# Optimization experiments

Hardware: AMD Instinct MI355X
Metric: run time of the kernel (lower is better)

Reference implementation:

```python
import jax, jax.numpy as jnp
import numpy as np

NUM_EMBEDDINGS = 4096
EMBEDDING_DIM = 512
N_TOKENS = 32768
COMMITMENT_COST = 0.25


def setup_inputs() -> dict:
    key = jax.random.key(0)
    k1, k2 = jax.random.split(key)
    flat_input = jax.random.normal(k1, (N_TOKENS, EMBEDDING_DIM), dtype=jnp.float32)
    # torch init: uniform(-1/K, 1/K)
    weight = jax.random.uniform(k2, (NUM_EMBEDDINGS, EMBEDDING_DIM), dtype=jnp.float32,
                                minval=-1.0 / NUM_EMBEDDINGS, maxval=1.0 / NUM_EMBEDDINGS)
    return {"flat_input": flat_input, "weight": weight}


def reference(flat_input, weight):
    distances = (jnp.sum(flat_input ** 2, axis=1, keepdims=True)
                 + jnp.sum(weight ** 2, axis=1)
                 - 2.0 * jnp.matmul(flat_input, weight.T))
    encoding_indices = jnp.argmin(distances, axis=1)  # [N]
    # one-hot @ weight == direct gather of codebook rows
    quantized = weight[encoding_indices]  # [N, D]

    e_latent_loss = jnp.mean((jax.lax.stop_gradient(quantized) - flat_input) ** 2, axis=1)
    q_latent_loss = jnp.mean((quantized - jax.lax.stop_gradient(flat_input)) ** 2, axis=1)
    loss = q_latent_loss + COMMITMENT_COST * e_latent_loss  # [N]

    # straight-through estimator
    quantized_st = flat_input + jax.lax.stop_gradient(quantized - flat_input)

    # avg_probs = mean of one-hot encodings over batch = normalized code counts
    counts = jnp.zeros((NUM_EMBEDDINGS,), dtype=flat_input.dtype).at[encoding_indices].add(1.0)
    avg_probs = counts / flat_input.shape[0]
    perplexity = jnp.exp(-jnp.sum(avg_probs * jnp.log(avg_probs + 1e-10)))

    return quantized_st, loss, perplexity, encoding_indices
```

## Files before the change

kernel.cpp:

```cpp
#include <hip/hip_runtime.h>
#include <math.h>

#define N_TOK 32768
#define K_CODES 4096
#define DIM 512
#define COMMIT 0.25f
#define NCAND 8
#define NSPLIT 2
#define SPLIT_CODES (K_CODES / NSPLIT)
#define NITER (SPLIT_CODES / 256)
#define BIAS 0.125f

typedef short s16x8 __attribute__((ext_vector_type(8)));
typedef float f32x4 __attribute__((ext_vector_type(4)));
typedef unsigned int uint32;
typedef unsigned long long u64;
typedef unsigned short u16;

__device__ __forceinline__ u16 f2bf(float f) {
    uint32 b = __float_as_uint(f);
    return (u16)((b + 0x7FFFu + ((b >> 16) & 1u)) >> 16);
}

__device__ __forceinline__ void gload16(const u16* g, u16* l) {
    __builtin_amdgcn_global_load_lds(
        (const __attribute__((address_space(1))) void*)g,
        (__attribute__((address_space(3))) void*)l,
        16, 0, 0);
}

__global__ __launch_bounds__(256) void tobf16_kernel(const float* __restrict__ src,
                                                     u16* __restrict__ dst, int n4) {
    int i = blockIdx.x * 256 + threadIdx.x;
    int stride = gridDim.x * 256;
    for (; i < n4; i += stride) {
        float4 v = ((const float4*)src)[i];
        ushort4 o;
        o.x = f2bf(v.x); o.y = f2bf(v.y); o.z = f2bf(v.z); o.w = f2bf(v.w);
        ((ushort4*)dst)[i] = o;
    }
}

__global__ __launch_bounds__(256) void rowsq_np_kernel(const float* __restrict__ a,
                                                       float* __restrict__ out,
                                                       int nrows) {
    #pragma clang fp contract(off)
    const int gw   = (blockIdx.x * 256 + threadIdx.x) >> 6;
    const int lane = threadIdx.x & 63;
    const int row  = gw * 8 + (lane >> 3);
    const int j    = lane & 7;
    if (row >= nrows) return;
    const float* p = a + (size_t)row * DIM;
    float blk[4];
    #pragma unroll
    for (int b = 0; b < 4; ++b) {
        const float* q = p + b * 128;
        float v = q[j];
        float r = v * v;
        for (int i = 8; i < 128; i += 8) { float u = q[i + j]; r += u * u; }
        float s1 = r  + __shfl_xor(r, 1);
        float s2 = s1 + __shfl_xor(s1, 2);
        float s3 = s2 + __shfl_xor(s2, 4);
        blk[b] = s3;
    }
    float res = (blk[0] + blk[1]) + (blk[2] + blk[3]);
    if (j == 0) out[row] = res;
}

__global__ __launch_bounds__(512, 2) void screen_kernel(const u16* __restrict__ xb,
                                                        const u16* __restrict__ wb,
                                                        const float* __restrict__ w2f,
                                                        u64* __restrict__ candPart) {
    __shared__ __attribute__((aligned(16))) u16 POOL[65536];

    const int tid  = threadIdx.x;
    const int wv   = tid >> 6;
    const int wt   = wv >> 1;
    const int wcc  = wv & 1;
    const int lane = tid & 63;
    const int quad = lane >> 4;
    const int n15  = lane & 15;
    const int m0   = blockIdx.x * 256;
    const int sbase = blockIdx.y * SPLIT_CODES;

    const int l8  = lane >> 3;
    const int qsw = (lane & 7) ^ l8;

    const u16* xg = xb + (size_t)(m0 + wv * 32 + l8) * DIM + qsw * 8;
    const u16* wit = wb + (size_t)(sbase + wv * 32 + l8) * DIM + qsw * 8;

    uint32 r1[16], r2[16];
    #pragma unroll
    for (int i = 0; i < 16; ++i) { r1[i] = 0xFFFFFFFFu; r2[i] = 0xFFFFFFFFu; }

    #pragma unroll
    for (int j = 0; j < 4; ++j) {
        gload16(xg + (size_t)(j * 8) * DIM, &POOL[wv * 2048 + j * 512]);
        gload16(wit + (size_t)(j * 8) * DIM, &POOL[32768 + wv * 2048 + j * 512]);
    }
    __syncthreads();

    for (int it = 0; it < NITER; ++it) {
        const int nbase = sbase + it * 256;

        float w2pb[8];
        #pragma unroll
        for (int c = 0; c < 8; ++c) w2pb[c] = w2f[nbase + wcc * 128 + c * 16 + n15] + BIAS;

        f32x4 acc[4][8];
        #pragma unroll
        for (int i = 0; i < 4; ++i)
            #pragma unroll
            for (int c = 0; c < 8; ++c) acc[i][c] = (f32x4){0.f, 0.f, 0.f, 0.f};

        for (int kc = 0; kc < 8; ++kc) {
            if (kc < 7) {
                const int nb = (kc + 1) & 1;
                const int ko = (kc + 1) * 64;
                #pragma unroll
                for (int j = 0; j < 4; ++j) {
                    gload16(xg + (size_t)(j * 8) * DIM + ko,
                            &POOL[nb * 16384 + wv * 2048 + j * 512]);
                    gload16(wit + (size_t)(j * 8) * DIM + ko,
                            &POOL[32768 + nb * 16384 + wv * 2048 + j * 512]);
                }
            } else if (it < NITER - 1) {
                const u16* wn = wit + (size_t)256 * DIM;
                #pragma unroll
                for (int j = 0; j < 4; ++j) {
                    gload16(xg + (size_t)(j * 8) * DIM, &POOL[wv * 2048 + j * 512]);
                    gload16(wn + (size_t)(j * 8) * DIM, &POOL[32768 + wv * 2048 + j * 512]);
                }
            }

            const u16* X = &POOL[(kc & 1) * 16384];
            const u16* W = &POOL[32768 + (kc & 1) * 16384];
            #pragma unroll
            for (int s = 0; s < 2; ++s) {
                const int qoff = ((s * 4 + quad) ^ (n15 & 7)) * 8;
                s16x8 af[4];
                #pragma unroll
                for (int i = 0; i < 4; ++i) {
                    const int tr = wt * 64 + i * 16 + n15;
                    af[i] = *(const s16x8*)&X[tr * 64 + qoff];
                }
                #pragma unroll
                for (int c = 0; c < 8; ++c) {
                    const int cr = wcc * 128 + c * 16 + n15;
                    s16x8 bf = *(const s16x8*)&W[cr * 64 + qoff];
                    #pragma unroll
                    for (int i = 0; i < 4; ++i)
                        acc[i][c] = __builtin_amdgcn_mfma_f32_16x16x32_bf16(af[i], bf, acc[i][c], 0, 0, 0);
                }
            }
            __syncthreads();
        }

        #pragma unroll
        for (int i = 0; i < 4; ++i)
            #pragma unroll
            for (int r = 0; r < 4; ++r) {
                const int ti = i * 4 + r;
                #pragma unroll
                for (int c = 0; c < 8; ++c) {
                    float s = fmaf(-2.0f, acc[i][c][r], w2pb[c]);
                    uint32 key = (__float_as_uint(s) & 0xFFFFFFC0u) | (uint32)((it << 3) | c);
                    uint32 mx = r1[ti] > key ? r1[ti] : key;
                    r1[ti] = r1[ti] < key ? r1[ti] : key;
                    r2[ti] = r2[ti] < mx ? r2[ti] : mx;
                }
            }
        wit += (size_t)256 * DIM;
    }

    u64* MS = (u64*)POOL;
    #pragma unroll
    for (int ti = 0; ti < 16; ++ti) {
        const int i = ti >> 2, r = ti & 3;
        const int tloc = wt * 64 + i * 16 + quad * 4 + r;
        #pragma unroll
        for (int e = 0; e < 2; ++e) {
            uint32 k  = e ? r2[ti] : r1[ti];
            uint32 vb = k & 0xFFFFFFC0u;
            uint32 id = k & 63u;
            uint32 code = (uint32)(sbase + (id >> 3) * 256 + wcc * 128 + (id & 7) * 16 + n15);
            MS[tloc * 64 + (wcc * 16 + n15) * 2 + e] = ((u64)vb << 32) | code;
        }
    }
    __syncthreads();
    if (tid < 256) {
        u64 best[6];
        #pragma unroll
        for (int c = 0; c < 6; ++c) best[c] = 0xFFFFFFFFFFFFFFFFull;
        for (int e = 0; e < 64; ++e) {
            u64 v = MS[tid * 64 + e];
            if (v < best[5]) {
                best[5] = v;
                #pragma unroll
                for (int p = 5; p > 0; --p)
                    if (best[p] < best[p - 1]) { u64 tv = best[p]; best[p] = best[p - 1]; best[p - 1] = tv; }
            }
        }
        const int token = m0 + tid;
        u64* dst = candPart + ((size_t)blockIdx.y * N_TOK + token) * 6;
        #pragma unroll
        for (int c = 0; c < 6; ++c) dst[c] = best[c];
    }
}

__global__ __launch_bounds__(256) void mergecand_kernel(const u64* __restrict__ candPart,
                                                        int* __restrict__ candF) {
    int t = blockIdx.x * 256 + threadIdx.x;
    u64 best[NCAND];
    #pragma unroll
    for (int c = 0; c < NCAND; ++c) best[c] = 0xFFFFFFFFFFFFFFFFull;
    for (int s = 0; s < NSPLIT; ++s) {
        const u64* src = candPart + ((size_t)s * N_TOK + t) * 6;
        #pragma unroll
        for (int c = 0; c < 6; ++c) {
            u64 v = src[c];
            if (v < best[NCAND - 1]) {
                best[NCAND - 1] = v;
                #pragma unroll
                for (int p = NCAND - 1; p > 0; --p)
                    if (best[p] < best[p - 1]) { u64 tv = best[p]; best[p] = best[p - 1]; best[p - 1] = tv; }
            }
        }
    }
    #pragma unroll
    for (int c = 0; c < NCAND; ++c) candF[(size_t)t * NCAND + c] = (int)(best[c] & 0xFFFu);
}

__global__ __launch_bounds__(256) void refine_kernel(const float* __restrict__ x,
                                                     const float* __restrict__ w,
                                                     const float* __restrict__ x2np,
                                                     const float* __restrict__ w2np,
                                                     const int* __restrict__ cand,
                                                     int* __restrict__ idx) {
    const int t    = blockIdx.x * 4 + (threadIdx.x >> 6);
    const int lane = threadIdx.x & 63;

    const float* xr = x + (size_t)t * DIM;
    float xv[8];
    #pragma unroll
    for (int j = 0; j < 8; ++j) xv[j] = xr[lane + 64 * j];
    const float x2 = x2np[t];

    float bd = 3.4e38f;
    int   bk = 0x7fffffff;
    for (int c = 0; c < NCAND; ++c) {
        int k = cand[(size_t)t * NCAND + c];
        const float* wr = w + (size_t)k * DIM;
        double m = 0.0;
        #pragma unroll
        for (int j = 0; j < 8; ++j)
            m = fma((double)xv[j], (double)wr[lane + 64 * j], m);
        #pragma unroll
        for (int off = 32; off >= 1; off >>= 1) m += __shfl_down(m, off);
        if (lane == 0) {
            #pragma clang fp contract(off)
            float m32 = (float)m;
            float T1  = x2 + w2np[k];
            float d   = T1 - 2.0f * m32;
            if (d < bd || (d == bd && k < bk)) { bd = d; bk = k; }
        }
    }
    if (lane == 0) idx[t] = bk;
}

__global__ __launch_bounds__(256) void gather_kernel(const float* __restrict__ x,
                                                     const float* __restrict__ w,
                                                     const int* __restrict__ idx,
                                                     float* __restrict__ out_q,
                                                     float* __restrict__ out_loss,
                                                     float* __restrict__ out_ind,
                                                     int* __restrict__ counts) {
    const int wave = threadIdx.x >> 6;
    const int lane = threadIdx.x & 63;
    const int token = blockIdx.x * 4 + wave;
    const int k = idx[token];

    const float4* xr = (const float4*)(x + (size_t)token * DIM);
    const float4* wr = (const float4*)(w + (size_t)k * DIM);
    float4*       qo = (float4*)(out_q + (size_t)token * DIM);

    float ss = 0.f;
    #pragma unroll
    for (int j = 0; j < 2; ++j) {
        int e = lane + j * 64;
        float4 xv = xr[e];
        float4 wv = wr[e];
        float4 d, o;
        d.x = wv.x - xv.x; o.x = xv.x + d.x;
        d.y = wv.y - xv.y; o.y = xv.y + d.y;
        d.z = wv.z - xv.z; o.z = xv.z + d.z;
        d.w = wv.w - xv.w; o.w = xv.w + d.w;
        ss += d.x * d.x + d.y * d.y + d.z * d.z + d.w * d.w;
        qo[e] = o;
    }
    #pragma unroll
    for (int off = 32; off >= 1; off >>= 1) ss += __shfl_down(ss, off);
    if (lane == 0) {
        float lm = ss * (1.0f / DIM);
        out_loss[token] = lm + COMMIT * lm;
        out_ind[token] = (float)k;
        atomicAdd(&counts[k], 1);
    }
}

__global__ __launch_bounds__(256) void perplex_kernel(const int* __restrict__ counts,
                                                      float* __restrict__ out2) {
    __shared__ double red[4];
    const int tid = threadIdx.x;
    const int lane = tid & 63;
    const int wid = tid >> 6;
    double s = 0.0;
    for (int t = tid; t < K_CODES; t += 256) {
        int c = counts[t];
        if (c) {
            double p = (double)c * (1.0 / N_TOK);
            s += p * log(p + 1e-10);
        }
    }
    #pragma unroll
    for (int off = 32; off >= 1; off >>= 1) s += __shfl_down(s, off);
    if (lane == 0) red[wid] = s;
    __syncthreads();
    if (tid == 0) {
        double t = red[0] + red[1] + red[2] + red[3];
        out2[0] = (float)exp(-t);
    }
}

extern "C" void kernel_launch(void* const* d_in, const int* in_sizes, int n_in,
                              void* d_out, int out_size, void* d_ws, size_t ws_size,
                              hipStream_t stream) {
    const float* x = (const float*)d_in[0];
    const float* w = (const float*)d_in[1];

    float* out0 = (float*)d_out;
    float* out1 = out0 + (size_t)N_TOK * DIM;
    float* out2 = out1 + N_TOK;
    float* out3 = out2 + 1;

    u64*   candPart = (u64*)d_ws;
    float* x2np     = (float*)(candPart + (size_t)NSPLIT * N_TOK * 6);
    float* w2np     = x2np + N_TOK;
    int*   idx      = (int*)(w2np + K_CODES);
    int*   counts   = idx + N_TOK;
    int*   candF    = counts + K_CODES;
    u16*   x_bf     = (u16*)(candF + (size_t)N_TOK * NCAND);
    u16*   w_bf     = x_bf + (size_t)N_TOK * DIM;

    hipMemsetAsync(counts, 0, K_CODES * sizeof(int), stream);

    tobf16_kernel<<<4096, 256, 0, stream>>>(x, x_bf, N_TOK * DIM / 4);
    tobf16_kernel<<<2048, 256, 0, stream>>>(w, w_bf, K_CODES * DIM / 4);
    rowsq_np_kernel<<<N_TOK / 32, 256, 0, stream>>>(x, x2np, N_TOK);
    rowsq_np_kernel<<<K_CODES / 32, 256, 0, stream>>>(w, w2np, K_CODES);
    screen_kernel<<<dim3(N_TOK / 256, NSPLIT), 512, 0, stream>>>(x_bf, w_bf, w2np, candPart);
    mergecand_kernel<<<N_TOK / 256, 256, 0, stream>>>(candPart, candF);
    refine_kernel<<<N_TOK / 4, 256, 0, stream>>>(x, w, x2np, w2np, candF, idx);
    gather_kernel<<<N_TOK / 4, 256, 0, stream>>>(x, w, idx, out0, out1, out3, counts);
    perplex_kernel<<<1, 256, 0, stream>>>(counts, out2);
}
```

Measured before the change: 510.3 us.

## Fuse prep kernels and merge/refine/gather; stage codebook norms in LDS

The bf16 conversion and row-norm computation are merged into one prep kernel per tensor. Candidate merging, exact refinement and gather/loss are fused into a single per-token kernel, which removes the candF/idx round-trips and two launches. The screen kernel now preloads biased codebook norms into extra LDS instead of reading them from global memory each iteration, and it changes the LDS swizzle index expression. The larger LDS footprint and launch bound of (512,1) may reduce blocks per CU.

```diff
diff --git a/kernel.cpp b/kernel.cpp
--- a/kernel.cpp
+++ b/kernel.cpp
@@ -29,28 +29,31 @@
         16, 0, 0);
 }
 
-__global__ __launch_bounds__(256) void tobf16_kernel(const float* __restrict__ src,
-                                                     u16* __restrict__ dst, int n4) {
-    int i = blockIdx.x * 256 + threadIdx.x;
-    int stride = gridDim.x * 256;
-    for (; i < n4; i += stride) {
-        float4 v = ((const float4*)src)[i];
-        ushort4 o;
-        o.x = f2bf(v.x); o.y = f2bf(v.y); o.z = f2bf(v.z); o.w = f2bf(v.w);
-        ((ushort4*)dst)[i] = o;
-    }
-}
-
-__global__ __launch_bounds__(256) void rowsq_np_kernel(const float* __restrict__ a,
-                                                       float* __restrict__ out,
-                                                       int nrows) {
+__global__ __launch_bounds__(256) void prep_kernel(const float* __restrict__ src,
+                                                   u16* __restrict__ bf,
+                                                   float* __restrict__ sq) {
     #pragma clang fp contract(off)
-    const int gw   = (blockIdx.x * 256 + threadIdx.x) >> 6;
-    const int lane = threadIdx.x & 63;
-    const int row  = gw * 8 + (lane >> 3);
+    const int tid  = threadIdx.x;
+    const int row0 = blockIdx.x * 32;
+
+    {
+        const float4* s4 = (const float4*)src + (size_t)row0 * 128;
+        ushort4*      d4 = (ushort4*)bf + (size_t)row0 * 128;
+        #pragma unroll
+        for (int i = 0; i < 16; ++i) {
+            int e = tid + i * 256;
+            float4 v = s4[e];
+            ushort4 o;
+            o.x = f2bf(v.x); o.y = f2bf(v.y); o.z = f2bf(v.z); o.w = f2bf(v.w);
+            d4[e] = o;
+        }
+    }
+
+    const int lane = tid & 63;
+    const int wvi  = tid >> 6;
+    const int row  = row0 + wvi * 8 + (lane >> 3);
     const int j    = lane & 7;
-    if (row >= nrows) return;
-    const float* p = a + (size_t)row * DIM;
+    const float* p = src + (size_t)row * DIM;
     float blk[4];
     #pragma unroll
     for (int b = 0; b < 4; ++b) {
@@ -64,14 +67,14 @@
         blk[b] = s3;
     }
     float res = (blk[0] + blk[1]) + (blk[2] + blk[3]);
-    if (j == 0) out[row] = res;
-}
-
-__global__ __launch_bounds__(512, 2) void screen_kernel(const u16* __restrict__ xb,
+    if (j == 0) sq[row] = res;
+}
+
+__global__ __launch_bounds__(512, 1) void screen_kernel(const u16* __restrict__ xb,
                                                         const u16* __restrict__ wb,
                                                         const float* __restrict__ w2f,
                                                         u64* __restrict__ candPart) {
-    __shared__ __attribute__((aligned(16))) u16 POOL[65536];
+    __shared__ __attribute__((aligned(16))) u16 POOL[69632];
 
     const int tid  = threadIdx.x;
     const int wv   = tid >> 6;
@@ -89,6 +92,12 @@
     const u16* xg = xb + (size_t)(m0 + wv * 32 + l8) * DIM + qsw * 8;
     const u16* wit = wb + (size_t)(sbase + wv * 32 + l8) * DIM + qsw * 8;
 
+    {
+        float* w2l = (float*)&POOL[65536];
+        for (int i = tid; i < SPLIT_CODES; i += 512)
+            w2l[i] = w2f[sbase + i] + BIAS;
+    }
+
     uint32 r1[16], r2[16];
     #pragma unroll
     for (int i = 0; i < 16; ++i) { r1[i] = 0xFFFFFFFFu; r2[i] = 0xFFFFFFFFu; }
@@ -101,12 +110,6 @@
     __syncthreads();
 
     for (int it = 0; it < NITER; ++it) {
-        const int nbase = sbase + it * 256;
-
-        float w2pb[8];
-        #pragma unroll
-        for (int c = 0; c < 8; ++c) w2pb[c] = w2f[nbase + wcc * 128 + c * 16 + n15] + BIAS;
-
         f32x4 acc[4][8];
         #pragma unroll
         for (int i = 0; i < 4; ++i)
@@ -137,17 +140,17 @@
             const u16* W = &POOL[32768 + (kc & 1) * 16384];
             #pragma unroll
             for (int s = 0; s < 2; ++s) {
-                const int qoff = ((s * 4 + quad) ^ (n15 & 7)) * 8;
+                const int lq = s * 4 + quad;
                 s16x8 af[4];
                 #pragma unroll
                 for (int i = 0; i < 4; ++i) {
                     const int tr = wt * 64 + i * 16 + n15;
-                    af[i] = *(const s16x8*)&X[tr * 64 + qoff];
+                    af[i] = *(const s16x8*)&X[tr * 64 + (lq ^ (tr & 7)) * 8];
                 }
                 #pragma unroll
                 for (int c = 0; c < 8; ++c) {
                     const int cr = wcc * 128 + c * 16 + n15;
-                    s16x8 bf = *(const s16x8*)&W[cr * 64 + qoff];
+                    s16x8 bf = *(const s16x8*)&W[cr * 64 + (lq ^ (cr & 7)) * 8];
                     #pragma unroll
                     for (int i = 0; i < 4; ++i)
                         acc[i][c] = __builtin_amdgcn_mfma_f32_16x16x32_bf16(af[i], bf, acc[i][c], 0, 0, 0);
@@ -156,6 +159,11 @@
             __syncthreads();
         }
 
+        const float* w2l = (const float*)&POOL[65536];
+        float w2pb[8];
+        #pragma unroll
+        for (int c = 0; c < 8; ++c)
+            w2pb[c] = w2l[it * 256 + wcc * 128 + c * 16 + n15];
         #pragma unroll
         for (int i = 0; i < 4; ++i)
             #pragma unroll
@@ -208,12 +216,19 @@
     }
 }
 
-__global__ __launch_bounds__(256) void mergecand_kernel(const u64* __restrict__ candPart,
-                                                        int* __restrict__ candF) {
-    int t = blockIdx.x * 256 + threadIdx.x;
+__global__ __launch_bounds__(256) void refine_gather_kernel(
+        const float* __restrict__ x, const float* __restrict__ w,
+        const float* __restrict__ x2np, const float* __restrict__ w2np,
+        const u64* __restrict__ candPart,
+        float* __restrict__ out_q, float* __restrict__ out_loss,
+        float* __restrict__ out_ind, int* __restrict__ counts) {
+    const int t    = blockIdx.x * 4 + (threadIdx.x >> 6);
+    const int lane = threadIdx.x & 63;
+
     u64 best[NCAND];
     #pragma unroll
     for (int c = 0; c < NCAND; ++c) best[c] = 0xFFFFFFFFFFFFFFFFull;
+    #pragma unroll
     for (int s = 0; s < NSPLIT; ++s) {
         const u64* src = candPart + ((size_t)s * N_TOK + t) * 6;
         #pragma unroll
@@ -227,18 +242,6 @@
             }
         }
     }
-    #pragma unroll
-    for (int c = 0; c < NCAND; ++c) candF[(size_t)t * NCAND + c] = (int)(best[c] & 0xFFFu);
-}
-
-__global__ __launch_bounds__(256) void refine_kernel(const float* __restrict__ x,
-                                                     const float* __restrict__ w,
-                                                     const float* __restrict__ x2np,
-                                                     const float* __restrict__ w2np,
-                                                     const int* __restrict__ cand,
-                                                     int* __restrict__ idx) {
-    const int t    = blockIdx.x * 4 + (threadIdx.x >> 6);
-    const int lane = threadIdx.x & 63;
 
     const float* xr = x + (size_t)t * DIM;
     float xv[8];
@@ -249,7 +252,7 @@
     float bd = 3.4e38f;
     int   bk = 0x7fffffff;
     for (int c = 0; c < NCAND; ++c) {
-        int k = cand[(size_t)t * NCAND + c];
+        int k = (int)(best[c] & 0xFFFu);
         const float* wr = w + (size_t)k * DIM;
         double m = 0.0;
         #pragma unroll
@@ -265,36 +268,23 @@
             if (d < bd || (d == bd && k < bk)) { bd = d; bk = k; }
         }
     }
-    if (lane == 0) idx[t] = bk;
-}
-
-__global__ __launch_bounds__(256) void gather_kernel(const float* __restrict__ x,
-                                                     const float* __restrict__ w,
-                                                     const int* __restrict__ idx,
-                                                     float* __restrict__ out_q,
-                                                     float* __restrict__ out_loss,
-                                                     float* __restrict__ out_ind,
-                                                     int* __restrict__ counts) {
-    const int wave = threadIdx.x >> 6;
-    const int lane = threadIdx.x & 63;
-    const int token = blockIdx.x * 4 + wave;
-    const int k = idx[token];
-
-    const float4* xr = (const float4*)(x + (size_t)token * DIM);
-    const float4* wr = (const float4*)(w + (size_t)k * DIM);
-    float4*       qo = (float4*)(out_q + (size_t)token * DIM);
+    const int kk = __shfl(bk, 0);
+
+    const float4* xr4 = (const float4*)(x + (size_t)t * DIM);
+    const float4* wr4 = (const float4*)(w + (size_t)kk * DIM);
+    float4*       qo  = (float4*)(out_q + (size_t)t * DIM);
 
     float ss = 0.f;
     #pragma unroll
     for (int j = 0; j < 2; ++j) {
         int e = lane + j * 64;
-        float4 xv = xr[e];
-        float4 wv = wr[e];
+        float4 xv4 = xr4[e];
+        float4 wv4 = wr4[e];
         float4 d, o;
-        d.x = wv.x - xv.x; o.x = xv.x + d.x;
-        d.y = wv.y - xv.y; o.y = xv.y + d.y;
-        d.z = wv.z - xv.z; o.z = xv.z + d.z;
-        d.w = wv.w - xv.w; o.w = xv.w + d.w;
+        d.x = wv4.x - xv4.x; o.x = xv4.x + d.x;
+        d.y = wv4.y - xv4.y; o.y = xv4.y + d.y;
+        d.z = wv4.z - xv4.z; o.z = xv4.z + d.z;
+        d.w = wv4.w - xv4.w; o.w = xv4.w + d.w;
         ss += d.x * d.x + d.y * d.y + d.z * d.z + d.w * d.w;
         qo[e] = o;
     }
@@ -302,9 +292,9 @@
     for (int off = 32; off >= 1; off >>= 1) ss += __shfl_down(ss, off);
     if (lane == 0) {
         float lm = ss * (1.0f / DIM);
-        out_loss[token] = lm + COMMIT * lm;
-        out_ind[token] = (float)k;
-        atomicAdd(&counts[k], 1);
+        out_loss[t] = lm + COMMIT * lm;
+        out_ind[t] = (float)kk;
+        atomicAdd(&counts[kk], 1);
     }
 }
 
@@ -354,13 +344,10 @@
 
     hipMemsetAsync(counts, 0, K_CODES * sizeof(int), stream);
 
-    tobf16_kernel<<<4096, 256, 0, stream>>>(x, x_bf, N_TOK * DIM / 4);
-    tobf16_kernel<<<2048, 256, 0, stream>>>(w, w_bf, K_CODES * DIM / 4);
-    rowsq_np_kernel<<<N_TOK / 32, 256, 0, stream>>>(x, x2np, N_TOK);
-    rowsq_np_kernel<<<K_CODES / 32, 256, 0, stream>>>(w, w2np, K_CODES);
+    prep_kernel<<<N_TOK / 32, 256, 0, stream>>>(x, x_bf, x2np);
+    prep_kernel<<<K_CODES / 32, 256, 0, stream>>>(w, w_bf, w2np);
     screen_kernel<<<dim3(N_TOK / 256, NSPLIT), 512, 0, stream>>>(x_bf, w_bf, w2np, candPart);
-    mergecand_kernel<<<N_TOK / 256, 256, 0, stream>>>(candPart, candF);
-    refine_kernel<<<N_TOK / 4, 256, 0, stream>>>(x, w, x2np, w2np, candF, idx);
-    gather_kernel<<<N_TOK / 4, 256, 0, stream>>>(x, w, idx, out0, out1, out3, counts);
+    refine_gather_kernel<<<N_TOK / 4, 256, 0, stream>>>(x, w, x2np, w2np, candPart,
+                                                        out0, out1, out3, counts);
     perplex_kernel<<<1, 256, 0, stream>>>(counts, out2);
 }
```

After: 433.1 us. -15.1%, faster.
